# Optimization experiments

Hardware: AMD Instinct MI355X
Metric: run time of the kernel (lower is better)

Reference implementation:

```python
import jax, jax.numpy as jnp
import numpy as np

D_MODEL, H, DK = 768, 12, 64
RQ, RK, RV = 6, 2, 2
B, S = 8, 4096


def setup_inputs() -> dict:
    key = jax.random.key(0)
    ks = jax.random.split(key, 16)
    def lin(k, din, dout):
        k1, k2 = jax.random.split(k)
        s = 1.0 / np.sqrt(din)
        W = jax.random.uniform(k1, (din, dout), jnp.float32, -s, s)
        b = jax.random.uniform(k2, (dout,), jnp.float32, -s, s)
        return W, b
    W_a_q, b_a_q = lin(ks[0], D_MODEL, H * RQ)
    W_b_q, b_b_q = lin(ks[1], D_MODEL, DK * RQ)
    W_a_k, b_a_k = lin(ks[2], D_MODEL, H * RK)
    W_b_k, b_b_k = lin(ks[3], D_MODEL, DK * RK)
    W_a_v, b_a_v = lin(ks[4], D_MODEL, H * RV)
    W_b_v, b_b_v = lin(ks[5], D_MODEL, DK * RV)
    W_out, b_out = lin(ks[6], H * DK, D_MODEL)
    x = jax.random.normal(ks[7], (B, S, D_MODEL), jnp.float32)
    rope_pos = jax.random.normal(ks[8], (S, DK), jnp.float32)
    return {
        "x": x, "rope_pos": rope_pos,
        "W_a_q": W_a_q, "b_a_q": b_a_q, "W_b_q": W_b_q, "b_b_q": b_b_q,
        "W_a_k": W_a_k, "b_a_k": b_a_k, "W_b_k": W_b_k, "b_b_k": b_b_k,
        "W_a_v": W_a_v, "b_a_v": b_a_v, "W_b_v": W_b_v, "b_b_v": b_b_v,
        "W_out": W_out, "b_out": b_out,
    }


def reference(x, rope_pos, W_a_q, b_a_q, W_b_q, b_b_q, W_a_k, b_a_k,
              W_b_k, b_b_k, W_a_v, b_a_v, W_b_v, b_b_v, W_out, b_out):
    b, s, _ = x.shape
    # factor projections; layout (B, S, rank, feature)
    A_Q = (x @ W_a_q + b_a_q).reshape(b, s, RQ, H)
    B_Q = (x @ W_b_q + b_b_q).reshape(b, s, RQ, DK)
    A_K = (x @ W_a_k + b_a_k).reshape(b, s, RK, H)
    B_K = (x @ W_b_k + b_b_k).reshape(b, s, RK, DK)
    A_V = (x @ W_a_v + b_a_v).reshape(b, s, RV, H)
    B_V = (x @ W_b_v + b_b_v).reshape(b, s, RV, DK)
    rope = rope_pos[None, :, None, :]  # (1,S,1,DK)
    B_Q = B_Q * rope
    B_K = B_K * rope
    # rank-sum outer products -> (B,S,H,DK)
    Q = jnp.einsum('bsrh,bsrd->bshd', A_Q, B_Q)
    K = jnp.einsum('bsrh,bsrd->bshd', A_K, B_K)
    V = jnp.einsum('bsrh,bsrd->bshd', A_V, B_V)
    # faithful to original: scores over head dim, shape (B,S,H,H)
    scores = jnp.einsum('bshd,bsgd->bshg', Q, K) / jnp.sqrt(jnp.float32(DK))
    attn = jax.nn.softmax(scores, axis=-1)
    out = jnp.einsum('bshg,bsgd->bshd', attn, V)  # (B,S,H,DK)
    # faithful reshape: (B,S,H,DK) -> transpose(1,2) -> (B,H,S,DK) -> view (B,S,H*DK)
    out = jnp.transpose(out, (0, 2, 1, 3)).reshape(b, s, H * DK)
    return out @ W_out + b_out
```

## Files before the change

kernel.cpp:

```cpp
#include <hip/hip_runtime.h>
#include <hip/hip_bf16.h>

#define D_MODEL 768
#define NH 12
#define DK 64
#define RQ 6
#define RK 2
#define RV 2
#define BATCH 8
#define SEQ 4096
#define NPOS (BATCH*SEQ)

typedef _Float16 v8h __attribute__((ext_vector_type(8)));
typedef float v4f __attribute__((ext_vector_type(4)));

__global__ __launch_bounds__(256) void repack(
    const float* __restrict__ Waq, const float* __restrict__ baq,
    const float* __restrict__ Wbq, const float* __restrict__ bbq,
    const float* __restrict__ Wak, const float* __restrict__ bak,
    const float* __restrict__ Wbk, const float* __restrict__ bbk,
    const float* __restrict__ Wav, const float* __restrict__ bav,
    const float* __restrict__ Wbv, const float* __restrict__ bbv,
    const float* __restrict__ Wo,
    _Float16* __restrict__ WcatT, _Float16* __restrict__ WoT,
    float* __restrict__ bcat)
{
    const int n = blockIdx.x;
    const int t = threadIdx.x;
    const float* W = nullptr; const float* bsrc = nullptr;
    int cols = 0, col = 0;
    if      (n <  72) { W=Waq; bsrc=baq; cols=72;  col=n;     }
    else if (n < 456) { W=Wbq; bsrc=bbq; cols=384; col=n-72;  }
    else if (n < 480) { W=Wak; bsrc=bak; cols=24;  col=n-456; }
    else if (n < 608) { W=Wbk; bsrc=bbk; cols=128; col=n-480; }
    else if (n < 632) { W=Wav; bsrc=bav; cols=24;  col=n-608; }
    else if (n < 760) { W=Wbv; bsrc=bbv; cols=128; col=n-632; }
    for (int k = t; k < 768; k += 256) {
        WcatT[(size_t)n*768 + k] = W ? (_Float16)W[(size_t)k*cols + col] : (_Float16)0.f;
        WoT[(size_t)n*768 + k]   = (_Float16)Wo[(size_t)k*768 + n];
    }
    if (t == 0) bcat[n] = W ? bsrc[col] : 0.f;
}

#define LSTR 129
template<int MODE>
__global__ __launch_bounds__(256) void mfma_gemm(
    const void* __restrict__ Aptr,
    const _Float16* __restrict__ BT,
    const float* __restrict__ bias,
    const float* __restrict__ rope,
    float* __restrict__ C)
{
    const int t = threadIdx.x;
    const int lane = t & 63;
    const int wave = t >> 6;

    const int flat = blockIdx.y * 6 + blockIdx.x;
    const int xcd = flat & 7;
    const int sub = flat >> 3;
    const int ct  = sub % 6;
    const int rt  = xcd * 32 + sub / 6;
    const int row0 = rt * 128;
    const int col0 = ct * 128;

    const int wrow = (wave >> 1) * 64;
    const int wcol = (wave & 1) * 64;

    __shared__ v8h As[4*LSTR];
    __shared__ v8h Bs[4*LSTR];

    v4f acc[4][4];
    #pragma unroll
    for (int i = 0; i < 4; ++i)
        #pragma unroll
        for (int j = 0; j < 4; ++j)
            acc[i][j] = (v4f){0.f, 0.f, 0.f, 0.f};

    const v8h* gB = (const v8h*)BT;
    const float4* gA32 = (const float4*)Aptr;
    const v8h* gA16 = (const v8h*)Aptr;

    const int arow = t >> 2;
    const int akc  = t & 3;

    const int q = lane >> 4;
    const int m = lane & 15;

    for (int k0 = 0; k0 < 768; k0 += 32) {
        __syncthreads();
        #pragma unroll
        for (int rh = 0; rh < 2; ++rh) {
            const int row = arow + rh*64;
            if (MODE == 0) {
                float4 f0 = gA32[(size_t)(row0 + row)*192 + (k0>>2) + akc*2];
                float4 f1 = gA32[(size_t)(row0 + row)*192 + (k0>>2) + akc*2 + 1];
                v8h h;
                h[0]=(_Float16)f0.x; h[1]=(_Float16)f0.y; h[2]=(_Float16)f0.z; h[3]=(_Float16)f0.w;
                h[4]=(_Float16)f1.x; h[5]=(_Float16)f1.y; h[6]=(_Float16)f1.z; h[7]=(_Float16)f1.w;
                As[akc*LSTR + row] = h;
            } else {
                As[akc*LSTR + row] = gA16[(size_t)(row0 + row)*96 + (k0>>3) + akc];
            }
            Bs[akc*LSTR + row] = gB[(size_t)(col0 + row)*96 + (k0>>3) + akc];
        }
        __syncthreads();

        v8h af[4], bf[4];
        #pragma unroll
        for (int mi = 0; mi < 4; ++mi)
            af[mi] = As[q*LSTR + wrow + mi*16 + m];
        #pragma unroll
        for (int ni = 0; ni < 4; ++ni)
            bf[ni] = Bs[q*LSTR + wcol + ni*16 + m];
        #pragma unroll
        for (int mi = 0; mi < 4; ++mi)
            #pragma unroll
            for (int ni = 0; ni < 4; ++ni)
                acc[mi][ni] = __builtin_amdgcn_mfma_f32_16x16x32_f16(
                    af[mi], bf[ni], acc[mi][ni], 0, 0, 0);
    }

    #pragma unroll
    for (int mi = 0; mi < 4; ++mi) {
        #pragma unroll
        for (int i = 0; i < 4; ++i) {
            const int grow = row0 + wrow + mi*16 + q*4 + i;
            #pragma unroll
            for (int ni = 0; ni < 4; ++ni) {
                const int gcol = col0 + wcol + ni*16 + m;
                float v = acc[mi][ni][i] + bias[gcol];
                if (MODE == 0) {
                    const int s = grow & 4095;
                    if (gcol >= 72 && gcol < 456)
                        v *= rope[s*64 + ((gcol - 72) & 63)];
                    else if (gcol >= 480 && gcol < 608)
                        v *= rope[s*64 + ((gcol - 480) & 63)];
                }
                C[(size_t)grow*768 + gcol] = v;
            }
        }
    }
}

__global__ __launch_bounds__(256) void tpa_attn_f(
    const float* __restrict__ P,
    _Float16* __restrict__ O)
{
    const int t = threadIdx.x;
    const int pos0 = blockIdx.x * 8;

    __shared__ float proj[8][772];
    __shared__ float Gs[8][12];
    __shared__ float sc[8][160];
    __shared__ float cs[8][24];

    const float4* gp = (const float4*)P;
    for (int i = t; i < 8*192; i += 256) {
        int p = i / 192, c = i - p*192;
        float4 u = gp[(size_t)(pos0 + p)*192 + c];
        proj[p][c*4+0] = u.x; proj[p][c*4+1] = u.y;
        proj[p][c*4+2] = u.z; proj[p][c*4+3] = u.w;
    }
    __syncthreads();

    if (t < 96) {
        int p = t / 12, u = t - (t/12)*12, r = u >> 1, r2 = u & 1;
        const float* bq = &proj[p][72  + r*64];
        const float* bk = &proj[p][480 + r2*64];
        const int ph = (r*8 + r2*16) & 63;
        float acc = 0.f;
        for (int i = 0; i < 64; ++i) {
            int d = (i + ph) & 63;
            acc = fmaf(bq[d], bk[d], acc);
        }
        Gs[p][u] = acc * 0.125f;
    }
    __syncthreads();

    for (int i = t; i < 8*144; i += 256) {
        int p = i / 144, v = i - p*144, h = v / 12, g = v - (v/12)*12;
        float s = 0.f;
        #pragma unroll
        for (int r = 0; r < RQ; ++r) {
            float mg = fmaf(Gs[p][r*2+1], proj[p][468 + g],
                            Gs[p][r*2+0] * proj[p][456 + g]);
            s = fmaf(proj[p][r*12 + h], mg, s);
        }
        sc[p][h*13 + g] = s;
    }
    __syncthreads();

    if (t < 96) {
        int p = t / 12, h = t - (t/12)*12;
        float* row = &sc[p][h*13];
        float mx = -1e30f;
        #pragma unroll
        for (int g = 0; g < NH; ++g) mx = fmaxf(mx, row[g]);
        float sum = 0.f;
        #pragma unroll
        for (int g = 0; g < NH; ++g) { float e = __expf(row[g]-mx); row[g] = e; sum += e; }
        float inv = 1.0f / sum;
        #pragma unroll
        for (int g = 0; g < NH; ++g) row[g] *= inv;
    }
    __syncthreads();

    if (t < 192) {
        int p = t / 24, u = t - (t/24)*24, h = u >> 1, r2 = u & 1;
        float acc = 0.f;
        #pragma unroll
        for (int g = 0; g < NH; ++g)
            acc = fmaf(sc[p][h*13+g], proj[p][608 + r2*12 + g], acc);
        cs[p][h*2 + r2] = acc;
    }
    __syncthreads();

    for (int i = t; i < 8*768; i += 256) {
        int p = i / 768, j = i - p*768, h = j >> 6, d = j & 63;
        int pos = pos0 + p, b = pos >> 12, s = pos & 4095;
        float val = fmaf(cs[p][h*2+1], proj[p][632 + 64 + d],
                         cs[p][h*2+0] * proj[p][632 + d]);
        O[(((size_t)b*NH + h)*SEQ + s)*DK + d] = (_Float16)val;
    }
}

extern "C" void kernel_launch(void* const* d_in, const int* in_sizes, int n_in,
                              void* d_out, int out_size, void* d_ws, size_t ws_size,
                              hipStream_t stream) {
    const float* x    = (const float*)d_in[0];
    const float* rope = (const float*)d_in[1];
    const float* Waq  = (const float*)d_in[2];
    const float* baq  = (const float*)d_in[3];
    const float* Wbq  = (const float*)d_in[4];
    const float* bbq  = (const float*)d_in[5];
    const float* Wak  = (const float*)d_in[6];
    const float* bak  = (const float*)d_in[7];
    const float* Wbk  = (const float*)d_in[8];
    const float* bbk  = (const float*)d_in[9];
    const float* Wav  = (const float*)d_in[10];
    const float* bav  = (const float*)d_in[11];
    const float* Wbv  = (const float*)d_in[12];
    const float* bbv  = (const float*)d_in[13];
    const float* Wo   = (const float*)d_in[14];
    const float* bo   = (const float*)d_in[15];

    char* ws = (char*)d_ws;
    _Float16* WcatT = (_Float16*)(ws);
    _Float16* WoT   = (_Float16*)(ws + 1179648);
    float*    bcat  = (float*)(ws + 2359296);
    _Float16* O     = (_Float16*)(ws + 2363392);

    float* P = (float*)d_out;

    repack<<<768, 256, 0, stream>>>(Waq, baq, Wbq, bbq, Wak, bak, Wbk, bbk,
                                    Wav, bav, Wbv, bbv, Wo, WcatT, WoT, bcat);

    dim3 gg(6, 256);
    mfma_gemm<0><<<gg, 256, 0, stream>>>(x, WcatT, bcat, rope, P);

    tpa_attn_f<<<NPOS/8, 256, 0, stream>>>(P, O);

    mfma_gemm<1><<<gg, 256, 0, stream>>>(O, WoT, bo, nullptr, (float*)d_out);
}
```

Baseline: 399.0 us.

## Pre-convert x to fp16 and stage GEMM tiles via direct global-to-LDS loads

Adds a separate kernel that converts x from fp32 to fp16 into the workspace buffer O, which is reused later for attention output. Both GEMMs now load A and B tiles straight into LDS with global_load_lds 16-byte transfers instead of going through registers, dropping the padded LDS stride. The aim is to cut VGPR traffic and load instruction overhead in the GEMM main loop. In exchange it adds an extra full pass over x (read fp32, write fp16), and the unpadded layout may cause LDS bank conflicts on the fragment reads.

```diff
diff --git a/kernel.cpp b/kernel.cpp
--- a/kernel.cpp
+++ b/kernel.cpp
@@ -13,6 +13,14 @@
 
 typedef _Float16 v8h __attribute__((ext_vector_type(8)));
 typedef float v4f __attribute__((ext_vector_type(4)));
+
+#define GLDS16(ldst, gsrc)                                                     \
+    __builtin_amdgcn_global_load_lds(                                          \
+        (const __attribute__((address_space(1))) void*)(unsigned long long)    \
+            (const void*)(gsrc),                                               \
+        (__attribute__((address_space(3))) void*)(unsigned int)                \
+            (unsigned long long)(void*)(ldst),                                 \
+        16, 0, 0)
 
 __global__ __launch_bounds__(256) void repack(
     const float* __restrict__ Waq, const float* __restrict__ baq,
@@ -42,10 +50,23 @@
     if (t == 0) bcat[n] = W ? bsrc[col] : 0.f;
 }
 
-#define LSTR 129
+__global__ __launch_bounds__(256) void convert_x(
+    const float4* __restrict__ x, v8h* __restrict__ xh)
+{
+    const int nth = gridDim.x * 256;
+    for (int i = blockIdx.x*256 + threadIdx.x; i < NPOS*96; i += nth) {
+        float4 a = x[2*(size_t)i];
+        float4 b = x[2*(size_t)i + 1];
+        v8h h;
+        h[0]=(_Float16)a.x; h[1]=(_Float16)a.y; h[2]=(_Float16)a.z; h[3]=(_Float16)a.w;
+        h[4]=(_Float16)b.x; h[5]=(_Float16)b.y; h[6]=(_Float16)b.z; h[7]=(_Float16)b.w;
+        xh[i] = h;
+    }
+}
+
 template<int MODE>
 __global__ __launch_bounds__(256) void mfma_gemm(
-    const void* __restrict__ Aptr,
+    const _Float16* __restrict__ A,
     const _Float16* __restrict__ BT,
     const float* __restrict__ bias,
     const float* __restrict__ rope,
@@ -66,8 +87,8 @@
     const int wrow = (wave >> 1) * 64;
     const int wcol = (wave & 1) * 64;
 
-    __shared__ v8h As[4*LSTR];
-    __shared__ v8h Bs[4*LSTR];
+    __shared__ v8h As[512];
+    __shared__ v8h Bs[512];
 
     v4f acc[4][4];
     #pragma unroll
@@ -76,42 +97,34 @@
         for (int j = 0; j < 4; ++j)
             acc[i][j] = (v4f){0.f, 0.f, 0.f, 0.f};
 
+    const v8h* gA = (const v8h*)A;
     const v8h* gB = (const v8h*)BT;
-    const float4* gA32 = (const float4*)Aptr;
-    const v8h* gA16 = (const v8h*)Aptr;
-
-    const int arow = t >> 2;
-    const int akc  = t & 3;
+
+    const int r  = t & 127;
+    const int kc = t >> 7;
+    const size_t gaBase = (size_t)(row0 + r)*96 + kc;
+    const size_t gbBase = (size_t)(col0 + r)*96 + kc;
+    char* ldsA = (char*)As + t*16;
+    char* ldsB = (char*)Bs + t*16;
 
     const int q = lane >> 4;
     const int m = lane & 15;
 
-    for (int k0 = 0; k0 < 768; k0 += 32) {
+    for (int k0 = 0; k0 < 96; k0 += 4) {
         __syncthreads();
-        #pragma unroll
-        for (int rh = 0; rh < 2; ++rh) {
-            const int row = arow + rh*64;
-            if (MODE == 0) {
-                float4 f0 = gA32[(size_t)(row0 + row)*192 + (k0>>2) + akc*2];
-                float4 f1 = gA32[(size_t)(row0 + row)*192 + (k0>>2) + akc*2 + 1];
-                v8h h;
-                h[0]=(_Float16)f0.x; h[1]=(_Float16)f0.y; h[2]=(_Float16)f0.z; h[3]=(_Float16)f0.w;
-                h[4]=(_Float16)f1.x; h[5]=(_Float16)f1.y; h[6]=(_Float16)f1.z; h[7]=(_Float16)f1.w;
-                As[akc*LSTR + row] = h;
-            } else {
-                As[akc*LSTR + row] = gA16[(size_t)(row0 + row)*96 + (k0>>3) + akc];
-            }
-            Bs[akc*LSTR + row] = gB[(size_t)(col0 + row)*96 + (k0>>3) + akc];
-        }
+        GLDS16(ldsA,        gA + gaBase + k0);
+        GLDS16(ldsA + 4096, gA + gaBase + k0 + 2);
+        GLDS16(ldsB,        gB + gbBase + k0);
+        GLDS16(ldsB + 4096, gB + gbBase + k0 + 2);
         __syncthreads();
 
         v8h af[4], bf[4];
         #pragma unroll
         for (int mi = 0; mi < 4; ++mi)
-            af[mi] = As[q*LSTR + wrow + mi*16 + m];
+            af[mi] = As[q*128 + wrow + mi*16 + m];
         #pragma unroll
         for (int ni = 0; ni < 4; ++ni)
-            bf[ni] = Bs[q*LSTR + wcol + ni*16 + m];
+            bf[ni] = Bs[q*128 + wcol + ni*16 + m];
         #pragma unroll
         for (int mi = 0; mi < 4; ++mi)
             #pragma unroll
@@ -252,11 +265,15 @@
 
     float* P = (float*)d_out;
 
+    _Float16* Xh = O;
+
     repack<<<768, 256, 0, stream>>>(Waq, baq, Wbq, bbq, Wak, bak, Wbk, bbk,
                                     Wav, bav, Wbv, bbv, Wo, WcatT, WoT, bcat);
 
+    convert_x<<<1024, 256, 0, stream>>>((const float4*)x, (v8h*)Xh);
+
     dim3 gg(6, 256);
-    mfma_gemm<0><<<gg, 256, 0, stream>>>(x, WcatT, bcat, rope, P);
+    mfma_gemm<0><<<gg, 256, 0, stream>>>(Xh, WcatT, bcat, rope, P);
 
     tpa_attn_f<<<NPOS/8, 256, 0, stream>>>(P, O);
 
```

Result: slower. 443.3 us (+11.1%).
